# Optimization experiments

Measured on AMD Instinct MI355X. Metric: run time of the kernel, lower is better.

Reference implementation:

```python
import jax, jax.numpy as jnp
import numpy as np

B, P, E, H = 32, 16, 50000, 128
EPS = 1e-5


def setup_inputs() -> dict:
    key = jax.random.key(0)
    ks = jax.random.split(key, 8)
    return {
        "inputs": jax.random.randint(ks[0], (B, P, E), 0, 2, dtype=jnp.int32),
        "emb": jax.random.normal(ks[1], (E, H), jnp.float32) * 0.02,
        "w1": jax.random.normal(ks[2], (H, H), jnp.float32) / np.sqrt(H),
        "b1": jax.random.normal(ks[3], (H,), jnp.float32) * 0.01,
        "w2": jax.random.normal(ks[4], (H, H), jnp.float32) / np.sqrt(H),
        "b2": jax.random.normal(ks[5], (H,), jnp.float32) * 0.01,
        "ln1_g": jnp.ones((H,), jnp.float32),
        "ln1_b": jnp.zeros((H,), jnp.float32),
        "ln2_g": jnp.ones((H,), jnp.float32),
        "ln2_b": jnp.zeros((H,), jnp.float32),
        "bn1_g": jnp.ones((H,), jnp.float32),
        "bn1_b": jnp.zeros((H,), jnp.float32),
        "bn2_g": jnp.ones((H,), jnp.float32),
        "bn2_b": jnp.zeros((H,), jnp.float32),
    }


def _layer_norm(x, g, b):
    mu = x.mean(-1, keepdims=True)
    var = ((x - mu) ** 2).mean(-1, keepdims=True)
    return g * (x - mu) / jnp.sqrt(var + EPS) + b


def _batch_norm_eval(x, g, b):
    # eval-mode BatchNorm1d with running_mean=0, running_var=1
    return g * x / jnp.sqrt(1.0 + EPS) + b


def reference(inputs, emb, w1, b1, w2, b2, ln1_g, ln1_b, ln2_g, ln2_b,
              bn1_g, bn1_b, bn2_g, bn2_b):
    # padding_idx=0: embedding row 0 is zero (but still counted in the mean,
    # matching the torch loop which averages over all selected indices)
    emb0 = emb.at[0].set(0.0)
    mask = (inputs == 1).astype(emb.dtype)            # [B, P, E] multi-hot
    sums = jnp.einsum("bpe,eh->bph", mask, emb0)       # segment-sum as one GEMM
    cnt = mask.sum(-1, keepdims=True)                  # [B, P, 1]
    path_emb = jnp.where(cnt > 0, sums / jnp.maximum(cnt, 1.0), 0.0)
    x = path_emb.mean(axis=1)                          # mean over paths -> [B, H]
    x = _layer_norm(x, ln1_g, ln1_b)
    x = jax.nn.relu(x @ w1.T + b1)
    x = _batch_norm_eval(x, bn1_g, bn1_b)              # dropout = identity (eval)
    x = _layer_norm(x, ln2_g, ln2_b)
    x = jax.nn.relu(x @ w2.T + b2)
    x = _batch_norm_eval(x, bn2_g, bn2_b)
    return x
```

## Files before the change

### kernel.cpp

```cpp
#include <hip/hip_runtime.h>
#include <stdint.h>

#define E_DIM 50000
#define EP    50048
#define HD    128
#define BD    32
#define PD    16
#define MD    512
#define BM    32
#define BK    64
#define KCHUNK 768
#define NKC   66
#define NST   12
#define EPSF  1e-5f

typedef short short8 __attribute__((ext_vector_type(8)));
typedef float f32x4  __attribute__((ext_vector_type(4)));

__device__ __forceinline__ uint16_t f2bf(float f) {
  uint32_t u = __float_as_uint(f);
  u += 0x7FFFu + ((u >> 16) & 1u);
  return (uint16_t)(u >> 16);
}

__global__ __launch_bounds__(256) void k_embF(const float* __restrict__ emb,
                                              uint16_t* __restrict__ embF) {
  __shared__ __align__(16) uint16_t lds[HD * 64];
  const int t  = threadIdx.x;
  const int e0 = blockIdx.x * 64;

#pragma unroll
  for (int pass = 0; pass < 8; ++pass) {
    const int el = pass * 8 + (t >> 5);
    const int h  = (t & 31) * 4;
    const int eg = e0 + el;
    float4 v = {0.f, 0.f, 0.f, 0.f};
    if (eg < E_DIM && eg != 0)
      v = *(const float4*)(emb + (size_t)eg * HD + h);
    const uint16_t q0 = f2bf(v.x), q1 = f2bf(v.y), q2 = f2bf(v.z), q3 = f2bf(v.w);
    lds[(h + 0) * 64 + (el ^ (((h + 0) & 7) << 3))] = q0;
    lds[(h + 1) * 64 + (el ^ (((h + 1) & 7) << 3))] = q1;
    lds[(h + 2) * 64 + (el ^ (((h + 2) & 7) << 3))] = q2;
    lds[(h + 3) * 64 + (el ^ (((h + 3) & 7) << 3))] = q3;
  }
  __syncthreads();

  const int w    = t >> 6;
  const int lane = t & 63;
  const int r16  = lane & 15;
  const int kgq  = (lane >> 4) * 8;
  uint16_t* outp = embF + (size_t)blockIdx.x * 8192 + (size_t)w * 2048 + lane * 8;
#pragma unroll
  for (int fr = 0; fr < 4; ++fr) {
    const int h  = (2 * w + (fr & 1)) * 16 + r16;
    const int el = (fr >> 1) * 32 + kgq;
    short8 d = *(const short8*)(lds + h * 64 + (el ^ ((h & 7) << 3)));
    *(short8*)(outp + fr * 512) = d;
  }
}

__global__ __launch_bounds__(256, 4) void k_gemm(const int* __restrict__ inp,
                                                 const uint16_t* __restrict__ embF,
                                                 float* __restrict__ part,
                                                 float* __restrict__ cntp) {
  __shared__ __align__(16) uint16_t ldsA[2][BM * BK];

  const int t    = threadIdx.x;
  const int lane = t & 63;
  const int w    = t >> 6;

  const int virt = (blockIdx.x & 7) * (NKC * 16 / 8) + (blockIdx.x >> 3);
  const int mb = virt & 15;
  const int kc = virt >> 4;
  const int e0 = kc * KCHUNK;
  const int nst = min(NST, (EP - e0) >> 6);

  const int sr = t >> 3;
  const int sc = (t & 7) * 8;
  const int* ap = inp + (size_t)(mb * BM + sr) * E_DIM + e0 + sc;
  const int aw = sr * 128 + (((t & 7) ^ (sr & 7)) << 4);

  const uint16_t* bp = embF + ((size_t)kc * NST) * 8192 + (size_t)w * 2048 + lane * 8;

  const int r16  = lane & 15;
  const int kg   = (lane >> 4) << 3;
  const int aoff = r16 * 128;
  const int swr  = r16 & 7;

  f32x4 acc00 = {0.f,0.f,0.f,0.f}, acc01 = {0.f,0.f,0.f,0.f};
  f32x4 acc10 = {0.f,0.f,0.f,0.f}, acc11 = {0.f,0.f,0.f,0.f};
  uint32_t cnt = 0;

  int4 aP0x, aP0y, aP1x, aP1y;
  short8 bP0[4], bP1[4];

#define LOAD_A(DSTX, DSTY, SIG)                                   \
  DSTX = (int4){0,0,0,0}; DSTY = (int4){0,0,0,0};                 \
  if (e0 + (SIG) * 64 + sc < E_DIM) {                             \
    DSTX = *(const int4*)(ap + (SIG) * 64);                       \
    DSTY = *(const int4*)(ap + (SIG) * 64 + 4);                   \
  }

#define LOAD_B(DST, SIG)                                          \
  _Pragma("unroll")                                               \
  for (int fr = 0; fr < 4; ++fr)                                  \
    DST[fr] = *(const short8*)(bp + (size_t)(SIG) * 8192 + fr * 512);

#define CONVERT_WRITE_A(SRCX, SRCY, BUF, SIG)                     \
  {                                                               \
    const uint32_t w01 = (uint32_t)SRCX.x | ((uint32_t)SRCX.y << 16); \
    const uint32_t w23 = (uint32_t)SRCX.z | ((uint32_t)SRCX.w << 16); \
    const uint32_t w45 = (uint32_t)SRCY.x | ((uint32_t)SRCY.y << 16); \
    const uint32_t w67 = (uint32_t)SRCY.z | ((uint32_t)SRCY.w << 16); \
    cnt += w01 + w23 + w45 + w67;                                 \
    uint4 d = { w01 * 0x3F80u, w23 * 0x3F80u, w45 * 0x3F80u, w67 * 0x3F80u }; \
    *(uint4*)((char*)ldsA[BUF] + aw) = d;                         \
  }

#define BARRIER()                                                 \
  asm volatile("s_waitcnt lgkmcnt(0)" ::: "memory");              \
  __builtin_amdgcn_s_barrier();                                   \
  __builtin_amdgcn_sched_barrier(0);

#define MFMA_STAGE(BUF, BREG)                                     \
  _Pragma("unroll")                                               \
  for (int kk = 0; kk < 2; ++kk) {                                \
    const int sw16 = (((kk * 4) + (kg >> 3)) ^ swr) << 4;         \
    const short8 af0 = *(const short8*)((const char*)ldsA[BUF] + aoff + sw16); \
    const short8 af1 = *(const short8*)((const char*)ldsA[BUF] + aoff + sw16 + 2048); \
    acc00 = __builtin_amdgcn_mfma_f32_16x16x32_bf16(af0, BREG[kk*2+0], acc00, 0, 0, 0); \
    acc01 = __builtin_amdgcn_mfma_f32_16x16x32_bf16(af0, BREG[kk*2+1], acc01, 0, 0, 0); \
    acc10 = __builtin_amdgcn_mfma_f32_16x16x32_bf16(af1, BREG[kk*2+0], acc10, 0, 0, 0); \
    acc11 = __builtin_amdgcn_mfma_f32_16x16x32_bf16(af1, BREG[kk*2+1], acc11, 0, 0, 0); \
  }

  LOAD_A(aP0x, aP0y, 0)
  LOAD_A(aP1x, aP1y, 1)
  LOAD_B(bP0, 0)
  CONVERT_WRITE_A(aP0x, aP0y, 0, 0)
  BARRIER()

  for (int s = 0; s < nst; s += 2) {
    if (s + 2 < nst) { LOAD_A(aP0x, aP0y, s + 2) }
    if (s + 1 < nst) { LOAD_B(bP1, s + 1) }
    MFMA_STAGE(0, bP0)
    if (s + 1 < nst) { CONVERT_WRITE_A(aP1x, aP1y, 1, s + 1) }
    BARRIER()

    if (s + 3 < nst) { LOAD_A(aP1x, aP1y, s + 3) }
    if (s + 2 < nst) { LOAD_B(bP0, s + 2) }
    if (s + 1 < nst) { MFMA_STAGE(1, bP1) }
    if (s + 2 < nst) { CONVERT_WRITE_A(aP0x, aP0y, 0, s + 2) }
    BARRIER()
  }

#undef LOAD_A
#undef LOAD_B
#undef CONVERT_WRITE_A
#undef BARRIER
#undef MFMA_STAGE

  {
    const int jr = (lane >> 4) << 2;
    float* pt0 = part + (size_t)kc * (MD * HD)
               + (size_t)(mb * BM + jr) * HD + w * 32 + r16;
#pragma unroll
    for (int j = 0; j < 4; ++j) {
      pt0[j * HD]             = acc00[j];
      pt0[j * HD + 16]        = acc01[j];
      pt0[(16 + j) * HD]      = acc10[j];
      pt0[(16 + j) * HD + 16] = acc11[j];
    }
  }

  {
    int c = (int)((cnt & 0xFFFFu) + (cnt >> 16));
    c += __shfl_xor(c, 1);
    c += __shfl_xor(c, 2);
    c += __shfl_xor(c, 4);
    if ((lane & 7) == 0)
      cntp[kc * MD + mb * BM + w * 8 + (lane >> 3)] = (float)c;
  }
}

__global__ __launch_bounds__(128) void k_reduce(const float* __restrict__ part,
                                                const float* __restrict__ cntp,
                                                float* __restrict__ pe) {
  const int r = blockIdx.x;
  const int t = threadIdx.x;
  const float* pp = part + (size_t)r * HD + t;
  float s = 0.f;
#pragma unroll 6
  for (int kc = 0; kc < NKC; ++kc) s += pp[(size_t)kc * (MD * HD)];
  float c = 0.f;
#pragma unroll 6
  for (int kc = 0; kc < NKC; ++kc) c += cntp[kc * MD + r];
  pe[r * HD + t] = (c > 0.f) ? (s / c) : 0.f;
}

__global__ __launch_bounds__(128) void k_tail(
    const float* __restrict__ pe,
    const float* __restrict__ w1, const float* __restrict__ b1,
    const float* __restrict__ w2, const float* __restrict__ b2,
    const float* __restrict__ ln1g, const float* __restrict__ ln1b,
    const float* __restrict__ ln2g, const float* __restrict__ ln2b,
    const float* __restrict__ bn1g, const float* __restrict__ bn1b,
    const float* __restrict__ bn2g, const float* __restrict__ bn2b,
    float* __restrict__ out) {
  const int b = blockIdx.x, t = threadIdx.x;
  __shared__ float sh[HD];
  __shared__ float red[HD];

  float x = 0.f;
#pragma unroll
  for (int p = 0; p < PD; ++p) x += pe[(b * PD + p) * HD + t];
  x *= (1.f / PD);

  const float bninv = rsqrtf(1.f + EPSF);

  red[t] = x; __syncthreads();
  for (int o = 64; o > 0; o >>= 1) { if (t < o) red[t] += red[t + o]; __syncthreads(); }
  const float mu1 = red[0] * (1.f / HD); __syncthreads();
  const float d1 = x - mu1;
  red[t] = d1 * d1; __syncthreads();
  for (int o = 64; o > 0; o >>= 1) { if (t < o) red[t] += red[t + o]; __syncthreads(); }
  const float v1 = red[0] * (1.f / HD); __syncthreads();
  const float y1 = ln1g[t] * d1 * rsqrtf(v1 + EPSF) + ln1b[t];

  sh[t] = y1; __syncthreads();
  float a = b1[t];
  const float4* wrow1 = (const float4*)(w1 + (size_t)t * HD);
#pragma unroll 8
  for (int k = 0; k < 32; ++k) {
    const float4 w = wrow1[k];
    a += w.x * sh[k * 4] + w.y * sh[k * 4 + 1] + w.z * sh[k * 4 + 2] + w.w * sh[k * 4 + 3];
  }
  a = fmaxf(a, 0.f);
  a = bn1g[t] * a * bninv + bn1b[t];
  __syncthreads();

  red[t] = a; __syncthreads();
  for (int o = 64; o > 0; o >>= 1) { if (t < o) red[t] += red[t + o]; __syncthreads(); }
  const float mu2 = red[0] * (1.f / HD); __syncthreads();
  const float d2 = a - mu2;
  red[t] = d2 * d2; __syncthreads();
  for (int o = 64; o > 0; o >>= 1) { if (t < o) red[t] += red[t + o]; __syncthreads(); }
  const float v2 = red[0] * (1.f / HD); __syncthreads();
  const float y2 = ln2g[t] * d2 * rsqrtf(v2 + EPSF) + ln2b[t];

  sh[t] = y2; __syncthreads();
  float a2 = b2[t];
  const float4* wrow2 = (const float4*)(w2 + (size_t)t * HD);
#pragma unroll 8
  for (int k = 0; k < 32; ++k) {
    const float4 w = wrow2[k];
    a2 += w.x * sh[k * 4] + w.y * sh[k * 4 + 1] + w.z * sh[k * 4 + 2] + w.w * sh[k * 4 + 3];
  }
  a2 = fmaxf(a2, 0.f);
  a2 = bn2g[t] * a2 * bninv + bn2b[t];
  out[b * HD + t] = a2;
}

extern "C" void kernel_launch(void* const* d_in, const int* in_sizes, int n_in,
                              void* d_out, int out_size, void* d_ws, size_t ws_size,
                              hipStream_t stream) {
  const int*   inp  = (const int*)d_in[0];
  const float* emb  = (const float*)d_in[1];
  const float* w1   = (const float*)d_in[2];
  const float* b1   = (const float*)d_in[3];
  const float* w2   = (const float*)d_in[4];
  const float* b2   = (const float*)d_in[5];
  const float* ln1g = (const float*)d_in[6];
  const float* ln1b = (const float*)d_in[7];
  const float* ln2g = (const float*)d_in[8];
  const float* ln2b = (const float*)d_in[9];
  const float* bn1g = (const float*)d_in[10];
  const float* bn1b = (const float*)d_in[11];
  const float* bn2g = (const float*)d_in[12];
  const float* bn2b = (const float*)d_in[13];
  float* out = (float*)d_out;

  char* ws = (char*)d_ws;
  uint16_t* embF = (uint16_t*)ws;
  float* part = (float*)(ws + 12976128);
  float* cntp = (float*)(ws + 12976128 + 17301504);
  float* pe   = (float*)(ws + 12976128 + 17301504 + 135168);

  k_embF<<<NKC * NST, 256, 0, stream>>>(emb, embF);
  k_gemm<<<NKC * 16, 256, 0, stream>>>(inp, embF, part, cntp);
  k_reduce<<<MD, 128, 0, stream>>>(part, cntp, pe);
  k_tail<<<BD, 128, 0, stream>>>(pe, w1, b1, w2, b2, ln1g, ln1b, ln2g, ln2b,
                                 bn1g, bn1b, bn2g, bn2b, out);
}
```

Measured before the change: 59.64 us.

## Deepen GEMM pipeline with fully unrolled 3-deep B prefetch and larger K chunks

Splits the K dimension into 46 chunks of 17 stages instead of 66 chunks of 12, which cuts the number of partial sums written and re-read by the reduction. The GEMM main loop is fully unrolled with four A register sets and three B register sets, so global loads are issued further ahead of their MFMA use, and s_setprio is raised around the MFMA groups. The reduce kernel now splits the K-chunk sum across four 128-thread groups and combines them through shared memory. The cost is more registers per thread, so occupancy is lowered to 3 waves per SIMD, and fewer GEMM blocks are launched.

```diff
diff --git a/kernel.cpp b/kernel.cpp
--- a/kernel.cpp
+++ b/kernel.cpp
@@ -9,9 +9,9 @@
 #define MD    512
 #define BM    32
 #define BK    64
-#define KCHUNK 768
-#define NKC   66
-#define NST   12
+#define KCHUNK 1088
+#define NKC   46
+#define NST   17
 #define EPSF  1e-5f
 
 typedef short short8 __attribute__((ext_vector_type(8)));
@@ -59,7 +59,7 @@
   }
 }
 
-__global__ __launch_bounds__(256, 4) void k_gemm(const int* __restrict__ inp,
+__global__ __launch_bounds__(256, 3) void k_gemm(const int* __restrict__ inp,
                                                  const uint16_t* __restrict__ embF,
                                                  float* __restrict__ part,
                                                  float* __restrict__ cntp) {
@@ -73,7 +73,6 @@
   const int mb = virt & 15;
   const int kc = virt >> 4;
   const int e0 = kc * KCHUNK;
-  const int nst = min(NST, (EP - e0) >> 6);
 
   const int sr = t >> 3;
   const int sc = (t & 7) * 8;
@@ -83,82 +82,97 @@
   const uint16_t* bp = embF + ((size_t)kc * NST) * 8192 + (size_t)w * 2048 + lane * 8;
 
   const int r16  = lane & 15;
-  const int kg   = (lane >> 4) << 3;
+  const int kg3  = (lane >> 4);
+  const int swr  = r16 & 7;
   const int aoff = r16 * 128;
-  const int swr  = r16 & 7;
+  const int o00 = aoff + ((kg3 ^ swr) << 4);
+  const int o01 = o00 + 2048;
+  const int o10 = aoff + (((4 + kg3) ^ swr) << 4);
+  const int o11 = o10 + 2048;
 
   f32x4 acc00 = {0.f,0.f,0.f,0.f}, acc01 = {0.f,0.f,0.f,0.f};
   f32x4 acc10 = {0.f,0.f,0.f,0.f}, acc11 = {0.f,0.f,0.f,0.f};
   uint32_t cnt = 0;
 
-  int4 aP0x, aP0y, aP1x, aP1y;
-  short8 bP0[4], bP1[4];
-
-#define LOAD_A(DSTX, DSTY, SIG)                                   \
-  DSTX = (int4){0,0,0,0}; DSTY = (int4){0,0,0,0};                 \
+  int4 a0x, a0y, a1x, a1y, a2x, a2y, a3x, a3y;
+  short8 t00, t01, t02, t03, t10, t11, t12, t13, t20, t21, t22, t23;
+
+#define LOAD_A(AX, AY, SIG)                                       \
+  AX = (int4){0,0,0,0}; AY = (int4){0,0,0,0};                     \
   if (e0 + (SIG) * 64 + sc < E_DIM) {                             \
-    DSTX = *(const int4*)(ap + (SIG) * 64);                       \
-    DSTY = *(const int4*)(ap + (SIG) * 64 + 4);                   \
-  }
-
-#define LOAD_B(DST, SIG)                                          \
-  _Pragma("unroll")                                               \
-  for (int fr = 0; fr < 4; ++fr)                                  \
-    DST[fr] = *(const short8*)(bp + (size_t)(SIG) * 8192 + fr * 512);
-
-#define CONVERT_WRITE_A(SRCX, SRCY, BUF, SIG)                     \
+    AX = *(const int4*)(ap + (SIG) * 64);                         \
+    AY = *(const int4*)(ap + (SIG) * 64 + 4);                     \
+  }
+
+#define LOAD_B4(B0_, B1_, B2_, B3_, SIG)                          \
+  B0_ = *(const short8*)(bp + (size_t)(SIG) * 8192);              \
+  B1_ = *(const short8*)(bp + (size_t)(SIG) * 8192 + 512);        \
+  B2_ = *(const short8*)(bp + (size_t)(SIG) * 8192 + 1024);       \
+  B3_ = *(const short8*)(bp + (size_t)(SIG) * 8192 + 1536);
+
+#define CW(AX, AY, BUF)                                           \
   {                                                               \
-    const uint32_t w01 = (uint32_t)SRCX.x | ((uint32_t)SRCX.y << 16); \
-    const uint32_t w23 = (uint32_t)SRCX.z | ((uint32_t)SRCX.w << 16); \
-    const uint32_t w45 = (uint32_t)SRCY.x | ((uint32_t)SRCY.y << 16); \
-    const uint32_t w67 = (uint32_t)SRCY.z | ((uint32_t)SRCY.w << 16); \
+    const uint32_t w01 = (uint32_t)AX.x | ((uint32_t)AX.y << 16); \
+    const uint32_t w23 = (uint32_t)AX.z | ((uint32_t)AX.w << 16); \
+    const uint32_t w45 = (uint32_t)AY.x | ((uint32_t)AY.y << 16); \
+    const uint32_t w67 = (uint32_t)AY.z | ((uint32_t)AY.w << 16); \
     cnt += w01 + w23 + w45 + w67;                                 \
     uint4 d = { w01 * 0x3F80u, w23 * 0x3F80u, w45 * 0x3F80u, w67 * 0x3F80u }; \
     *(uint4*)((char*)ldsA[BUF] + aw) = d;                         \
   }
 
-#define BARRIER()                                                 \
+#define BAR()                                                     \
   asm volatile("s_waitcnt lgkmcnt(0)" ::: "memory");              \
   __builtin_amdgcn_s_barrier();                                   \
   __builtin_amdgcn_sched_barrier(0);
 
-#define MFMA_STAGE(BUF, BREG)                                     \
-  _Pragma("unroll")                                               \
-  for (int kk = 0; kk < 2; ++kk) {                                \
-    const int sw16 = (((kk * 4) + (kg >> 3)) ^ swr) << 4;         \
-    const short8 af0 = *(const short8*)((const char*)ldsA[BUF] + aoff + sw16); \
-    const short8 af1 = *(const short8*)((const char*)ldsA[BUF] + aoff + sw16 + 2048); \
-    acc00 = __builtin_amdgcn_mfma_f32_16x16x32_bf16(af0, BREG[kk*2+0], acc00, 0, 0, 0); \
-    acc01 = __builtin_amdgcn_mfma_f32_16x16x32_bf16(af0, BREG[kk*2+1], acc01, 0, 0, 0); \
-    acc10 = __builtin_amdgcn_mfma_f32_16x16x32_bf16(af1, BREG[kk*2+0], acc10, 0, 0, 0); \
-    acc11 = __builtin_amdgcn_mfma_f32_16x16x32_bf16(af1, BREG[kk*2+1], acc11, 0, 0, 0); \
-  }
-
-  LOAD_A(aP0x, aP0y, 0)
-  LOAD_A(aP1x, aP1y, 1)
-  LOAD_B(bP0, 0)
-  CONVERT_WRITE_A(aP0x, aP0y, 0, 0)
-  BARRIER()
-
-  for (int s = 0; s < nst; s += 2) {
-    if (s + 2 < nst) { LOAD_A(aP0x, aP0y, s + 2) }
-    if (s + 1 < nst) { LOAD_B(bP1, s + 1) }
-    MFMA_STAGE(0, bP0)
-    if (s + 1 < nst) { CONVERT_WRITE_A(aP1x, aP1y, 1, s + 1) }
-    BARRIER()
-
-    if (s + 3 < nst) { LOAD_A(aP1x, aP1y, s + 3) }
-    if (s + 2 < nst) { LOAD_B(bP0, s + 2) }
-    if (s + 1 < nst) { MFMA_STAGE(1, bP1) }
-    if (s + 2 < nst) { CONVERT_WRITE_A(aP0x, aP0y, 0, s + 2) }
-    BARRIER()
-  }
+#define MFMA4(BUF, B0_, B1_, B2_, B3_)                            \
+  {                                                               \
+    const char* Ab = (const char*)ldsA[BUF];                      \
+    const short8 af0 = *(const short8*)(Ab + o00);                \
+    const short8 af1 = *(const short8*)(Ab + o01);                \
+    const short8 ag0 = *(const short8*)(Ab + o10);                \
+    const short8 ag1 = *(const short8*)(Ab + o11);                \
+    __builtin_amdgcn_s_setprio(1);                                \
+    acc00 = __builtin_amdgcn_mfma_f32_16x16x32_bf16(af0, B0_, acc00, 0, 0, 0); \
+    acc01 = __builtin_amdgcn_mfma_f32_16x16x32_bf16(af0, B1_, acc01, 0, 0, 0); \
+    acc10 = __builtin_amdgcn_mfma_f32_16x16x32_bf16(af1, B0_, acc10, 0, 0, 0); \
+    acc11 = __builtin_amdgcn_mfma_f32_16x16x32_bf16(af1, B1_, acc11, 0, 0, 0); \
+    acc00 = __builtin_amdgcn_mfma_f32_16x16x32_bf16(ag0, B2_, acc00, 0, 0, 0); \
+    acc01 = __builtin_amdgcn_mfma_f32_16x16x32_bf16(ag0, B3_, acc01, 0, 0, 0); \
+    acc10 = __builtin_amdgcn_mfma_f32_16x16x32_bf16(ag1, B2_, acc10, 0, 0, 0); \
+    acc11 = __builtin_amdgcn_mfma_f32_16x16x32_bf16(ag1, B3_, acc11, 0, 0, 0); \
+    __builtin_amdgcn_s_setprio(0);                                \
+  }
+
+  LOAD_A(a0x, a0y, 0) LOAD_A(a1x, a1y, 1) LOAD_A(a2x, a2y, 2) LOAD_A(a3x, a3y, 3)
+  LOAD_B4(t00, t01, t02, t03, 0) LOAD_B4(t10, t11, t12, t13, 1)
+  CW(a0x, a0y, 0)
+  BAR()
+
+   LOAD_A(a0x,a0y,4)  LOAD_B4(t20,t21,t22,t23,2)  MFMA4(0, t00,t01,t02,t03) CW(a1x,a1y,1) BAR()
+   LOAD_A(a1x,a1y,5)  LOAD_B4(t00,t01,t02,t03,3)  MFMA4(1, t10,t11,t12,t13) CW(a2x,a2y,0) BAR()
+   LOAD_A(a2x,a2y,6)  LOAD_B4(t10,t11,t12,t13,4)  MFMA4(0, t20,t21,t22,t23) CW(a3x,a3y,1) BAR()
+   LOAD_A(a3x,a3y,7)  LOAD_B4(t20,t21,t22,t23,5)  MFMA4(1, t00,t01,t02,t03) CW(a0x,a0y,0) BAR()
+   LOAD_A(a0x,a0y,8)  LOAD_B4(t00,t01,t02,t03,6)  MFMA4(0, t10,t11,t12,t13) CW(a1x,a1y,1) BAR()
+   LOAD_A(a1x,a1y,9)  LOAD_B4(t10,t11,t12,t13,7)  MFMA4(1, t20,t21,t22,t23) CW(a2x,a2y,0) BAR()
+   LOAD_A(a2x,a2y,10) LOAD_B4(t20,t21,t22,t23,8)  MFMA4(0, t00,t01,t02,t03) CW(a3x,a3y,1) BAR()
+   LOAD_A(a3x,a3y,11) LOAD_B4(t00,t01,t02,t03,9)  MFMA4(1, t10,t11,t12,t13) CW(a0x,a0y,0) BAR()
+   LOAD_A(a0x,a0y,12) LOAD_B4(t10,t11,t12,t13,10) MFMA4(0, t20,t21,t22,t23) CW(a1x,a1y,1) BAR()
+   LOAD_A(a1x,a1y,13) LOAD_B4(t20,t21,t22,t23,11) MFMA4(1, t00,t01,t02,t03) CW(a2x,a2y,0) BAR()
+   LOAD_A(a2x,a2y,14) LOAD_B4(t00,t01,t02,t03,12) MFMA4(0, t10,t11,t12,t13) CW(a3x,a3y,1) BAR()
+   LOAD_A(a3x,a3y,15) LOAD_B4(t10,t11,t12,t13,13) MFMA4(1, t20,t21,t22,t23) CW(a0x,a0y,0) BAR()
+   LOAD_A(a0x,a0y,16) LOAD_B4(t20,t21,t22,t23,14) MFMA4(0, t00,t01,t02,t03) CW(a1x,a1y,1) BAR()
+                      LOAD_B4(t00,t01,t02,t03,15) MFMA4(1, t10,t11,t12,t13) CW(a2x,a2y,0) BAR()
+                      LOAD_B4(t10,t11,t12,t13,16) MFMA4(0, t20,t21,t22,t23) CW(a3x,a3y,1) BAR()
+                                                  MFMA4(1, t00,t01,t02,t03) CW(a0x,a0y,0) BAR()
+                                                  MFMA4(0, t10,t11,t12,t13)
 
 #undef LOAD_A
-#undef LOAD_B
-#undef CONVERT_WRITE_A
-#undef BARRIER
-#undef MFMA_STAGE
+#undef LOAD_B4
+#undef CW
+#undef BAR
+#undef MFMA4
 
   {
     const int jr = (lane >> 4) << 2;
@@ -183,19 +197,33 @@
   }
 }
 
-__global__ __launch_bounds__(128) void k_reduce(const float* __restrict__ part,
+__global__ __launch_bounds__(512) void k_reduce(const float* __restrict__ part,
                                                 const float* __restrict__ cntp,
                                                 float* __restrict__ pe) {
-  const int r = blockIdx.x;
-  const int t = threadIdx.x;
-  const float* pp = part + (size_t)r * HD + t;
+  __shared__ float red[512];
+  __shared__ float cred[4];
+  const int r   = blockIdx.x;
+  const int t   = threadIdx.x;
+  const int col = t & 127;
+  const int sub = t >> 7;
+  const int k0  = (sub < 2) ? sub * 12 : 24 + (sub - 2) * 11;
+  const int kn  = (sub < 2) ? 12 : 11;
+  const float* pp = part + (size_t)(k0) * (MD * HD) + (size_t)r * HD + col;
   float s = 0.f;
-#pragma unroll 6
-  for (int kc = 0; kc < NKC; ++kc) s += pp[(size_t)kc * (MD * HD)];
-  float c = 0.f;
-#pragma unroll 6
-  for (int kc = 0; kc < NKC; ++kc) c += cntp[kc * MD + r];
-  pe[r * HD + t] = (c > 0.f) ? (s / c) : 0.f;
+#pragma unroll 4
+  for (int i = 0; i < kn; ++i) s += pp[(size_t)i * (MD * HD)];
+  red[t] = s;
+  if (col == 0) {
+    float c = 0.f;
+    for (int i = 0; i < kn; ++i) c += cntp[(k0 + i) * MD + r];
+    cred[sub] = c;
+  }
+  __syncthreads();
+  if (t < 128) {
+    const float tot = red[t] + red[t + 128] + red[t + 256] + red[t + 384];
+    const float c   = cred[0] + cred[1] + cred[2] + cred[3];
+    pe[r * HD + t] = (c > 0.f) ? (tot / c) : 0.f;
+  }
 }
 
 __global__ __launch_bounds__(128) void k_tail(
@@ -282,13 +310,13 @@
 
   char* ws = (char*)d_ws;
   uint16_t* embF = (uint16_t*)ws;
-  float* part = (float*)(ws + 12976128);
-  float* cntp = (float*)(ws + 12976128 + 17301504);
-  float* pe   = (float*)(ws + 12976128 + 17301504 + 135168);
+  float* part = (float*)(ws + 12812288);
+  float* cntp = (float*)(ws + 12812288 + 12058624);
+  float* pe   = (float*)(ws + 12812288 + 12058624 + 94208);
 
   k_embF<<<NKC * NST, 256, 0, stream>>>(emb, embF);
   k_gemm<<<NKC * 16, 256, 0, stream>>>(inp, embF, part, cntp);
-  k_reduce<<<MD, 128, 0, stream>>>(part, cntp, pe);
+  k_reduce<<<MD, 512, 0, stream>>>(part, cntp, pe);
   k_tail<<<BD, 128, 0, stream>>>(pe, w1, b1, w2, b2, ln1g, ln1b, ln2g, ln2b,
                                  bn1g, bn1b, bn2g, bn2b, out);
 }
```

Measured after the change: 60.53 us. About the same (+1.5%).
